# Optimization experiments

Hardware: AMD Instinct MI355X
Metric: run time of the kernel (lower is better)

## Reference

```python
import jax, jax.numpy as jnp
import numpy as np

ALPHA = 5.0   # ATan surrogate sharpness
THETA = 1.0   # firing threshold
EPS = 1e-5    # BatchNorm eps

@jax.custom_vjp
def spike(x):
    # forward: heaviside; backward: ATan surrogate
    return (x >= 0.0).astype(x.dtype)

def _spike_fwd(x):
    return spike(x), x

def _spike_bwd(x, g):
    return (g * (ALPHA / 2.0) / (1.0 + (jnp.pi / 2.0 * ALPHA * x) ** 2),)

spike.defvjp(_spike_fwd, _spike_bwd)

def lif_layer(x, W, beta_p, gamma, bias, U0):
    # x: [B,T,J], W: [I,J] -> h: [B,T,I]
    h = jnp.einsum('btj,ij->bti', x, W)
    # BatchNorm1d in training mode: per-channel stats over B*T (biased var)
    mu = h.mean(axis=(0, 1))
    var = h.var(axis=(0, 1))
    h = (h - mu) * jax.lax.rsqrt(var + EPS) * gamma + bias
    beta = jax.nn.sigmoid(beta_p)  # [I]
    S0 = jnp.zeros_like(U0)

    def step(carry, xt):
        Ut, St = carry
        Ut = beta * (Ut - THETA * St) + (1.0 - beta) * xt  # soft reset
        St = spike(Ut - THETA)
        return (Ut, St), St

    _, o = jax.lax.scan(step, (U0, S0), jnp.swapaxes(h, 0, 1))  # [T,B,I]
    return jnp.swapaxes(o, 0, 1)  # [B,T,I]

def setup_inputs() -> dict:
    key = jax.random.key(0)
    B, T, J, H = 32, 1024, 1024, 2048
    ks = jax.random.split(key, 16)
    f32 = jnp.float32
    inp = {
        'x': jax.random.normal(ks[0], (B, T, J), f32),
        'W1': jax.random.normal(ks[1], (H, J), f32) / np.sqrt(J),
        'beta1': jax.random.uniform(ks[2], (H,), f32, 0.0, 4.0),
        'gamma1': jnp.ones((H,), f32),
        'bias1': jnp.zeros((H,), f32),
        'U01': jax.random.uniform(ks[3], (B, H), f32),
        'W2': jax.random.normal(ks[4], (H, H), f32) / np.sqrt(H),
        'beta2': jax.random.uniform(ks[5], (H,), f32, 0.0, 4.0),
        'gamma2': jnp.ones((H,), f32),
        'bias2': jnp.zeros((H,), f32),
        'U02': jax.random.uniform(ks[6], (B, H), f32),
        'W3': jax.random.normal(ks[7], (J, H), f32) / np.sqrt(H),
        'beta3': jax.random.uniform(ks[8], (J,), f32, 0.0, 4.0),
        'gamma3': jnp.ones((J,), f32),
        'bias3': jnp.zeros((J,), f32),
        'U03': jax.random.uniform(ks[9], (B, J), f32),
    }
    return inp

def reference(x, W1, beta1, gamma1, bias1, U01,
              W2, beta2, gamma2, bias2, U02,
              W3, beta3, gamma3, bias3, U03):
    h = lif_layer(x, W1, beta1, gamma1, bias1, U01)
    h = lif_layer(h, W2, beta2, gamma2, bias2, U02)
    h = lif_layer(h, W3, beta3, gamma3, bias3, U03)
    return h
```

## Files before the change

### kernel.cpp

```cpp
#include <hip/hip_runtime.h>
#include <hip/hip_bf16.h>
#include <cmath>

#define BB 32
#define TT 1024
#define JJ 1024
#define HH 2048
#define MM (BB * TT)
#define MHALF (MM / 2)

typedef short s8v __attribute__((ext_vector_type(8)));
typedef float f4v __attribute__((ext_vector_type(4)));
typedef unsigned int u4v __attribute__((ext_vector_type(4)));
union ABu { u4v u; s8v v; };

__device__ inline void split_bf16x3(float w, unsigned short& h,
                                    unsigned short& m, unsigned short& l) {
    __hip_bfloat16 bh = __float2bfloat16(w);
    const float fh = __bfloat162float(bh);
    const float r1 = w - fh;
    __hip_bfloat16 bm = __float2bfloat16(r1);
    const float fm = __bfloat162float(bm);
    __hip_bfloat16 bl = __float2bfloat16(r1 - fm);
    h = *(unsigned short*)&bh; m = *(unsigned short*)&bm; l = *(unsigned short*)&bl;
}

__global__ void split_w(const float* __restrict__ W,
                        unsigned short* __restrict__ ph,
                        unsigned short* __restrict__ pm,
                        unsigned short* __restrict__ pl, int n)
{
    const int i = blockIdx.x * 256 + threadIdx.x;
    if (i >= n) return;
    split_bf16x3(W[i], ph[i], pm[i], pl[i]);
}

__global__ __launch_bounds__(256) void mfma_spk_gemm(
    const unsigned char* __restrict__ S,
    const unsigned short* __restrict__ Wh,
    const unsigned short* __restrict__ Wm,
    const unsigned short* __restrict__ Wl,
    float* __restrict__ C, int M, int N, int K)
{
    __shared__ __align__(16) unsigned short Blds[3][2][128][32];
    const int tid = threadIdx.x;
    const int wv = tid >> 6;
    const int lane = tid & 63;
    const int wm = wv >> 1, wn = wv & 1;
    const int r16 = lane & 15, quad = lane >> 4;
    const int bm = blockIdx.x * 128;
    const int bn = blockIdx.y * 128;
    const int Kb = K >> 3;

    f4v acc[4][4] = {};

    const int rl = lane >> 2, chl = lane & 3;
    size_t soff[2];
    int ldsrow[2];
#pragma unroll
    for (int i = 0; i < 2; ++i) {
        const int r = wv * 32 + i * 16 + rl;
        const int kc = (chl - (r >> 1)) & 3;
        soff[i] = (size_t)(bn + r) * K + kc * 8;
        ldsrow[i] = wv * 32 + i * 16;
    }

    size_t aoff[4];
#pragma unroll
    for (int ms = 0; ms < 4; ++ms)
        aoff[ms] = (size_t)(bm + wm * 64 + ms * 16 + r16) * Kb + quad;

    int bR[4], bC[4];
#pragma unroll
    for (int ns = 0; ns < 4; ++ns) {
        bR[ns] = wn * 64 + ns * 16 + r16;
        bC[ns] = ((quad + (bR[ns] >> 1)) & 3) * 8;
    }

    unsigned int ab[2][4];
#pragma unroll
    for (int kh = 0; kh < 2; ++kh)
#pragma unroll
        for (int ms = 0; ms < 4; ++ms) ab[kh][ms] = S[aoff[ms] + kh * 4];

    for (int k0 = 0; k0 < K; k0 += 64) {
        __syncthreads();
#pragma unroll
        for (int i = 0; i < 2; ++i)
#pragma unroll
            for (int kh = 0; kh < 2; ++kh) {
                __builtin_amdgcn_global_load_lds(
                    (const __attribute__((address_space(1))) void*)(Wh + soff[i] + k0 + kh * 32),
                    (__attribute__((address_space(3))) void*)&Blds[0][kh][ldsrow[i]][0], 16, 0, 0);
                __builtin_amdgcn_global_load_lds(
                    (const __attribute__((address_space(1))) void*)(Wm + soff[i] + k0 + kh * 32),
                    (__attribute__((address_space(3))) void*)&Blds[1][kh][ldsrow[i]][0], 16, 0, 0);
                __builtin_amdgcn_global_load_lds(
                    (const __attribute__((address_space(1))) void*)(Wl + soff[i] + k0 + kh * 32),
                    (__attribute__((address_space(3))) void*)&Blds[2][kh][ldsrow[i]][0], 16, 0, 0);
            }
        s8v afr[2][4];
#pragma unroll
        for (int kh = 0; kh < 2; ++kh)
#pragma unroll
            for (int ms = 0; ms < 4; ++ms) {
                ABu t;
                const unsigned int b = ab[kh][ms];
                t.u[0] = ((b        & 1u) * 0x3F80u) | (((b >> 1) & 1u) * 0x3F800000u);
                t.u[1] = (((b >> 2) & 1u) * 0x3F80u) | (((b >> 3) & 1u) * 0x3F800000u);
                t.u[2] = (((b >> 4) & 1u) * 0x3F80u) | (((b >> 5) & 1u) * 0x3F800000u);
                t.u[3] = (((b >> 6) & 1u) * 0x3F80u) | (((b >> 7) & 1u) * 0x3F800000u);
                afr[kh][ms] = t.v;
            }
        if (k0 + 64 < K) {
            const size_t kb = (size_t)((k0 + 64) >> 3);
#pragma unroll
            for (int kh = 0; kh < 2; ++kh)
#pragma unroll
                for (int ms = 0; ms < 4; ++ms) ab[kh][ms] = S[aoff[ms] + kb + kh * 4];
        }
        __syncthreads();
#pragma unroll
        for (int p = 0; p < 3; ++p)
#pragma unroll
            for (int kh = 0; kh < 2; ++kh) {
                s8v bf[4];
#pragma unroll
                for (int ns = 0; ns < 4; ++ns)
                    bf[ns] = *(const s8v*)&Blds[p][kh][bR[ns]][bC[ns]];
#pragma unroll
                for (int ms = 0; ms < 4; ++ms)
#pragma unroll
                    for (int ns = 0; ns < 4; ++ns)
                        acc[ms][ns] = __builtin_amdgcn_mfma_f32_16x16x32_bf16(
                            afr[kh][ms], bf[ns], acc[ms][ns], 0, 0, 0);
            }
    }

#pragma unroll
    for (int ms = 0; ms < 4; ++ms)
#pragma unroll
        for (int ns = 0; ns < 4; ++ns) {
            const int row = bm + wm * 64 + ms * 16 + quad * 4;
            const int col = bn + wn * 64 + ns * 16 + r16;
#pragma unroll
            for (int r = 0; r < 4; ++r)
                C[(size_t)(row + r) * N + col] = acc[ms][ns][r];
        }
}

struct Sp3 { unsigned int o0, o1, o2; };

__device__ inline Sp3 split_pair(float x, float y)
{
    const unsigned int xb = __float_as_uint(x), yb = __float_as_uint(y);
    const unsigned int x0 = xb & 0xFFFF0000u,  y0 = yb & 0xFFFF0000u;
    const float xr1 = x - __uint_as_float(x0), yr1 = y - __uint_as_float(y0);
    const unsigned int x1b = __float_as_uint(xr1), y1b = __float_as_uint(yr1);
    const unsigned int x1 = x1b & 0xFFFF0000u, y1 = y1b & 0xFFFF0000u;
    const float xr2 = xr1 - __uint_as_float(x1), yr2 = yr1 - __uint_as_float(y1);
    Sp3 r;
    r.o0 = __builtin_amdgcn_perm(yb, xb, 0x07060302u);
    r.o1 = __builtin_amdgcn_perm(y1b, x1b, 0x07060302u);
    r.o2 = __builtin_amdgcn_perm(__float_as_uint(yr2), __float_as_uint(xr2), 0x07060302u);
    return r;
}

__global__ __launch_bounds__(256) void mfma_f32x3_gemm(
    const float* __restrict__ A,
    const unsigned short* __restrict__ Wh,
    const unsigned short* __restrict__ Wm,
    const unsigned short* __restrict__ Wl,
    float* __restrict__ C, int M, int N, int K)
{
    __shared__ __align__(16) unsigned short Blds[3][2][128][32];
    const int tid = threadIdx.x;
    const int wv = tid >> 6;
    const int lane = tid & 63;
    const int wm = wv >> 1, wn = wv & 1;
    const int r16 = lane & 15, quad = lane >> 4;

    const int lin = blockIdx.y * 16 + blockIdx.x;
    const int ppx = gridDim.y >> 3;
    const int xcd = lin & 7, li = lin >> 3;
    const int pm = xcd * ppx + (li >> 4);
    const int pn = li & 15;
    const int bm = pm * 128;
    const int bn = pn * 128;

    f4v acc[4][4] = {};

    const int rl = lane >> 2, chl = lane & 3;
    size_t soff[2];
    int ldsrow[2];
#pragma unroll
    for (int i = 0; i < 2; ++i) {
        const int r = wv * 32 + i * 16 + rl;
        const int kc = (chl - (r >> 1)) & 3;
        soff[i] = (size_t)(bn + r) * K + kc * 8;
        ldsrow[i] = wv * 32 + i * 16;
    }

    size_t aoff[4];
#pragma unroll
    for (int ms = 0; ms < 4; ++ms)
        aoff[ms] = (size_t)(bm + wm * 64 + ms * 16 + r16) * K + quad * 8;

    int bR[4], bC[4];
#pragma unroll
    for (int ns = 0; ns < 4; ++ns) {
        bR[ns] = wn * 64 + ns * 16 + r16;
        bC[ns] = ((quad + (bR[ns] >> 1)) & 3) * 8;
    }

    float4 av[2][4][2];
#pragma unroll
    for (int kh = 0; kh < 2; ++kh)
#pragma unroll
        for (int ms = 0; ms < 4; ++ms) {
            av[kh][ms][0] = *(const float4*)(A + aoff[ms] + kh * 32);
            av[kh][ms][1] = *(const float4*)(A + aoff[ms] + kh * 32 + 4);
        }

    for (int k0 = 0; k0 < K; k0 += 64) {
        __syncthreads();
#pragma unroll
        for (int i = 0; i < 2; ++i)
#pragma unroll
            for (int kh = 0; kh < 2; ++kh) {
                __builtin_amdgcn_global_load_lds(
                    (const __attribute__((address_space(1))) void*)(Wh + soff[i] + k0 + kh * 32),
                    (__attribute__((address_space(3))) void*)&Blds[0][kh][ldsrow[i]][0], 16, 0, 0);
                __builtin_amdgcn_global_load_lds(
                    (const __attribute__((address_space(1))) void*)(Wm + soff[i] + k0 + kh * 32),
                    (__attribute__((address_space(3))) void*)&Blds[1][kh][ldsrow[i]][0], 16, 0, 0);
                __builtin_amdgcn_global_load_lds(
                    (const __attribute__((address_space(1))) void*)(Wl + soff[i] + k0 + kh * 32),
                    (__attribute__((address_space(3))) void*)&Blds[2][kh][ldsrow[i]][0], 16, 0, 0);
            }
        s8v afr[3][2][4];
#pragma unroll
        for (int kh = 0; kh < 2; ++kh)
#pragma unroll
            for (int ms = 0; ms < 4; ++ms) {
                ABu t0, t1, t2;
                const float4 v0 = av[kh][ms][0];
                const float4 v1 = av[kh][ms][1];
                const Sp3 s0 = split_pair(v0.x, v0.y);
                const Sp3 s1 = split_pair(v0.z, v0.w);
                const Sp3 s2 = split_pair(v1.x, v1.y);
                const Sp3 s3 = split_pair(v1.z, v1.w);
                t0.u[0] = s0.o0; t1.u[0] = s0.o1; t2.u[0] = s0.o2;
                t0.u[1] = s1.o0; t1.u[1] = s1.o1; t2.u[1] = s1.o2;
                t0.u[2] = s2.o0; t1.u[2] = s2.o1; t2.u[2] = s2.o2;
                t0.u[3] = s3.o0; t1.u[3] = s3.o1; t2.u[3] = s3.o2;
                afr[0][kh][ms] = t0.v;
                afr[1][kh][ms] = t1.v;
                afr[2][kh][ms] = t2.v;
            }
        __syncthreads();
        if (k0 + 64 < K) {
#pragma unroll
            for (int kh = 0; kh < 2; ++kh)
#pragma unroll
                for (int ms = 0; ms < 4; ++ms) {
                    av[kh][ms][0] = *(const float4*)(A + aoff[ms] + k0 + 64 + kh * 32);
                    av[kh][ms][1] = *(const float4*)(A + aoff[ms] + k0 + 64 + kh * 32 + 4);
                }
        }
#pragma unroll
        for (int kh = 0; kh < 2; ++kh)
#pragma unroll
            for (int pw = 0; pw < 3; ++pw) {
                s8v bf[4];
#pragma unroll
                for (int ns = 0; ns < 4; ++ns)
                    bf[ns] = *(const s8v*)&Blds[pw][kh][bR[ns]][bC[ns]];
#pragma unroll
                for (int pa = 0; pa + pw < 3; ++pa)
#pragma unroll
                    for (int ms = 0; ms < 4; ++ms)
#pragma unroll
                        for (int ns = 0; ns < 4; ++ns)
                            acc[ms][ns] = __builtin_amdgcn_mfma_f32_16x16x32_bf16(
                                afr[pa][kh][ms], bf[ns], acc[ms][ns], 0, 0, 0);
            }
    }

#pragma unroll
    for (int ms = 0; ms < 4; ++ms)
#pragma unroll
        for (int ns = 0; ns < 4; ++ns) {
            const int row = bm + wm * 64 + ms * 16 + quad * 4;
            const int col = bn + wn * 64 + ns * 16 + r16;
#pragma unroll
            for (int r = 0; r < 4; ++r)
                C[(size_t)(row + r) * N + col] = acc[ms][ns][r];
        }
}

#define RCHUNK 128

__global__ void bn_stats_partial2(const float* __restrict__ hA,
                                  const float* __restrict__ hB,
                                  float* __restrict__ partial, int N)
{
    const int n = blockIdx.x * 256 + threadIdx.x;
    const int chunk = blockIdx.y;
    const int half = (MM / RCHUNK) / 2;
    const float* __restrict__ h = (chunk < half) ? hA : hB;
    const int cl = chunk & (half - 1);
    const float* p = h + (size_t)cl * RCHUNK * N + n;
    float s = 0.f, s2 = 0.f;
#pragma unroll 4
    for (int r = 0; r < RCHUNK; ++r) {
        const float v = p[(size_t)r * N];
        s += v;
        s2 = fmaf(v, v, s2);
    }
    partial[((size_t)chunk * 2 + 0) * N + n] = s;
    partial[((size_t)chunk * 2 + 1) * N + n] = s2;
}

__global__ void bn_stats_final(const float* __restrict__ partial,
                               float* __restrict__ stats,
                               int N, int nchunks)
{
    const int n = blockIdx.x * 256 + threadIdx.x;
    double s = 0.0, s2 = 0.0;
    for (int c = 0; c < nchunks; ++c) {
        s  += (double)partial[((size_t)c * 2 + 0) * N + n];
        s2 += (double)partial[((size_t)c * 2 + 1) * N + n];
    }
    const double inv_m = 1.0 / (double)MM;
    const double mu = s * inv_m;
    const double var = s2 * inv_m - mu * mu;
    stats[n]     = (float)mu;
    stats[N + n] = (float)(1.0 / sqrt(var + 1e-5));
}

#define LIF_STEP_PACK(hv)                                            \
    do {                                                             \
        const float hn = ((hv) - mu) * rstd * g + bi;                \
        u = beta * (u - s) + omb * hn;                               \
        const bool sp = (u - 1.0f) >= 0.f;                           \
        s = sp ? 1.f : 0.f;                                          \
        const unsigned long long mball = __ballot(sp);               \
        if (lead) bits[widx] = mball;                                \
        widx += nw;                                                  \
    } while (0)

#define LIF_LOAD8(buf, tbase)                                        \
    _Pragma("unroll")                                                \
    for (int j = 0; j < 8; ++j) {                                    \
        const int tl = (tbase) + j;                                  \
        buf[j] = h[base + (size_t)(tl < TT ? tl : TT - 1) * N];      \
    }

__global__ __launch_bounds__(64) void bn_lif_scan_pack2(
    const float* __restrict__ hA,
    const float* __restrict__ hB,
    unsigned long long* __restrict__ bits,
    const float* __restrict__ stats,
    const float* __restrict__ gamma,
    const float* __restrict__ bias,
    const float* __restrict__ beta_p,
    const float* __restrict__ U0,
    int N)
{
    const int n = blockIdx.x * 64 + threadIdx.x;
    const int b = blockIdx.y;
    const float* __restrict__ h = (b < BB / 2) ? hA : hB;
    const int bl = b & (BB / 2 - 1);
    const int nw = N >> 6;
    const float mu = stats[n];
    const float rstd = stats[N + n];
    const float g = gamma[n];
    const float bi = bias[n];
    const float beta = 1.f / (1.f + expf(-beta_p[n]));
    const float omb = 1.f - beta;
    float u = U0[(size_t)b * N + n];
    float s = 0.f;
    const size_t base = ((size_t)bl * TT) * N + n;
    size_t widx = ((size_t)b * TT) * nw + (n >> 6);
    const bool lead = (threadIdx.x & 63) == 0;

    float b0[8], b1[8], b2[8], b3[8];
    LIF_LOAD8(b0, 0);
    LIF_LOAD8(b1, 8);
    LIF_LOAD8(b2, 16);
    for (int t0 = 0; t0 < TT; t0 += 32) {
        LIF_LOAD8(b3, t0 + 24);
#pragma unroll
        for (int j = 0; j < 8; ++j) { const float hv = b0[j]; LIF_STEP_PACK(hv); }
        LIF_LOAD8(b0, t0 + 32);
#pragma unroll
        for (int j = 0; j < 8; ++j) { const float hv = b1[j]; LIF_STEP_PACK(hv); }
        LIF_LOAD8(b1, t0 + 40);
#pragma unroll
        for (int j = 0; j < 8; ++j) { const float hv = b2[j]; LIF_STEP_PACK(hv); }
        LIF_LOAD8(b2, t0 + 48);
#pragma unroll
        for (int j = 0; j < 8; ++j) { const float hv = b3[j]; LIF_STEP_PACK(hv); }
    }
}

#define LIF_STEP_F32(hv)                                             \
    do {                                                             \
        const float hn = ((hv) - mu) * rstd * g + bi;                \
        u = beta * (u - s) + omb * hn;                               \
        s = ((u - 1.0f) >= 0.f) ? 1.f : 0.f;                         \
        out[oidx] = s;                                               \
        oidx += N;                                                   \
    } while (0)

__global__ __launch_bounds__(64) void bn_lif_scan_f32_2(
    const float* __restrict__ h,
    float* __restrict__ out,
    const float* __restrict__ stats,
    const float* __restrict__ gamma,
    const float* __restrict__ bias,
    const float* __restrict__ beta_p,
    const float* __restrict__ U0,
    int N)
{
    const int n = blockIdx.x * 64 + threadIdx.x;
    const int b = blockIdx.y;
    const float mu = stats[n];
    const float rstd = stats[N + n];
    const float g = gamma[n];
    const float bi = bias[n];
    const float beta = 1.f / (1.f + expf(-beta_p[n]));
    const float omb = 1.f - beta;
    float u = U0[(size_t)b * N + n];
    float s = 0.f;
    const size_t base = ((size_t)b * TT) * N + n;
    size_t oidx = base;

    float b0[8], b1[8], b2[8], b3[8];
    LIF_LOAD8(b0, 0);
    LIF_LOAD8(b1, 8);
    LIF_LOAD8(b2, 16);
    for (int t0 = 0; t0 < TT; t0 += 32) {
        LIF_LOAD8(b3, t0 + 24);
#pragma unroll
        for (int j = 0; j < 8; ++j) { const float hv = b0[j]; LIF_STEP_F32(hv); }
        LIF_LOAD8(b0, t0 + 32);
#pragma unroll
        for (int j = 0; j < 8; ++j) { const float hv = b1[j]; LIF_STEP_F32(hv); }
        LIF_LOAD8(b1, t0 + 40);
#pragma unroll
        for (int j = 0; j < 8; ++j) { const float hv = b2[j]; LIF_STEP_F32(hv); }
        LIF_LOAD8(b2, t0 + 48);
#pragma unroll
        for (int j = 0; j < 8; ++j) { const float hv = b3[j]; LIF_STEP_F32(hv); }
    }
}

extern "C" void kernel_launch(void* const* d_in, const int* in_sizes, int n_in,
                              void* d_out, int out_size, void* d_ws, size_t ws_size,
                              hipStream_t stream)
{
    const float* x   = (const float*)d_in[0];
    const float* W1  = (const float*)d_in[1];
    const float* bp1 = (const float*)d_in[2];
    const float* g1  = (const float*)d_in[3];
    const float* bi1 = (const float*)d_in[4];
    const float* U01 = (const float*)d_in[5];
    const float* W2  = (const float*)d_in[6];
    const float* bp2 = (const float*)d_in[7];
    const float* g2  = (const float*)d_in[8];
    const float* bi2 = (const float*)d_in[9];
    const float* U02 = (const float*)d_in[10];
    const float* W3  = (const float*)d_in[11];
    const float* bp3 = (const float*)d_in[12];
    const float* g3  = (const float*)d_in[13];
    const float* bi3 = (const float*)d_in[14];
    const float* U03 = (const float*)d_in[15];
    float* out = (float*)d_out;

    unsigned char* ws = (unsigned char*)d_ws;
    const size_t HA_BYTES  = (size_t)MHALF * HH * sizeof(float);
    const size_t SPK_BYTES = (size_t)MM * (HH / 8);
    float*              hA   = (float*)ws;
    float*              hB   = (float*)d_out;
    unsigned long long* spk  = (unsigned long long*)(ws + HA_BYTES);
    float*              part = (float*)(ws + HA_BYTES + SPK_BYTES);
    float*              stat = (float*)(ws + HA_BYTES + SPK_BYTES + 4194304);
    unsigned short*     W2h  = (unsigned short*)(ws + HA_BYTES + SPK_BYTES + 4194304 + 16384);
    unsigned short*     W2m  = W2h + (size_t)HH * HH;
    unsigned short*     W2l  = W2m + (size_t)HH * HH;
    unsigned short*     W3h  = W2l + (size_t)HH * HH;
    unsigned short*     W3m  = W3h + (size_t)JJ * HH;
    unsigned short*     W3l  = W3m + (size_t)JJ * HH;

    const dim3 blk(256);
    const dim3 blk64(64);
    const int nck = MM / RCHUNK;

    split_w<<<dim3((HH * JJ) / 256), blk, 0, stream>>>(W1, W2h, W2m, W2l, HH * JJ);
    mfma_f32x3_gemm<<<dim3(HH / 128, MHALF / 128), blk, 0, stream>>>(
        x, W2h, W2m, W2l, hA, MHALF, HH, JJ);
    mfma_f32x3_gemm<<<dim3(HH / 128, MHALF / 128), blk, 0, stream>>>(
        x + (size_t)MHALF * JJ, W2h, W2m, W2l, hB, MHALF, HH, JJ);
    split_w<<<dim3((HH * HH) / 256), blk, 0, stream>>>(W2, W2h, W2m, W2l, HH * HH);
    split_w<<<dim3((JJ * HH) / 256), blk, 0, stream>>>(W3, W3h, W3m, W3l, JJ * HH);

    bn_stats_partial2<<<dim3(HH / 256, nck), blk, 0, stream>>>(hA, hB, part, HH);
    bn_stats_final<<<dim3(HH / 256), blk, 0, stream>>>(part, stat, HH, nck);
    bn_lif_scan_pack2<<<dim3(HH / 64, BB), blk64, 0, stream>>>(
        hA, hB, spk, stat, g1, bi1, bp1, U01, HH);

    mfma_spk_gemm<<<dim3(MHALF / 128, HH / 128), blk, 0, stream>>>(
        (const unsigned char*)spk, W2h, W2m, W2l, hA, MHALF, HH, HH);
    mfma_spk_gemm<<<dim3(MHALF / 128, HH / 128), blk, 0, stream>>>(
        (const unsigned char*)spk + (size_t)MHALF * (HH / 8), W2h, W2m, W2l, hB, MHALF, HH, HH);
    bn_stats_partial2<<<dim3(HH / 256, nck), blk, 0, stream>>>(hA, hB, part, HH);
    bn_stats_final<<<dim3(HH / 256), blk, 0, stream>>>(part, stat, HH, nck);
    bn_lif_scan_pack2<<<dim3(HH / 64, BB), blk64, 0, stream>>>(
        hA, hB, spk, stat, g2, bi2, bp2, U02, HH);

    mfma_spk_gemm<<<dim3(MM / 128, JJ / 128), blk, 0, stream>>>(
        (const unsigned char*)spk, W3h, W3m, W3l, hA, MM, JJ, HH);
    bn_stats_partial2<<<dim3(JJ / 256, nck), blk, 0, stream>>>(
        hA, hA + (size_t)MHALF * JJ, part, JJ);
    bn_stats_final<<<dim3(JJ / 256), blk, 0, stream>>>(part, stat, JJ, nck);
    bn_lif_scan_f32_2<<<dim3(JJ / 64, BB), blk64, 0, stream>>>(
        hA, out, stat, g3, bi3, bp3, U03, JJ);
}
```

Measured before the change: 2.792 ms.

## Double-buffer weight tiles and enlarge spike GEMM block to 256 rows with 8 waves

The spike GEMM now uses 512 threads, so each block covers 256 M rows and eight waves share one 128-column weight tile, halving how often each weight tile is loaded. Weight slices are double-buffered in LDS and the next k-step is issued with global_load_lds during the current MFMAs. One of the two barriers per iteration is removed, and s_setprio raises wave priority around the MFMA bursts. The cost is twice the LDS footprint (48KB), possibly lower occupancy, and a reliance on a single barrier being enough to order the asynchronous LDS loads.

After: 2.703 ms. 1.03x faster.

```diff
diff --git a/kernel.cpp b/kernel.cpp
--- a/kernel.cpp
+++ b/kernel.cpp
@@ -35,35 +35,30 @@
     split_bf16x3(W[i], ph[i], pm[i], pl[i]);
 }
 
-__global__ __launch_bounds__(256) void mfma_spk_gemm(
+__global__ __launch_bounds__(512) void mfma_spk_gemm(
     const unsigned char* __restrict__ S,
     const unsigned short* __restrict__ Wh,
     const unsigned short* __restrict__ Wm,
     const unsigned short* __restrict__ Wl,
     float* __restrict__ C, int M, int N, int K)
 {
-    __shared__ __align__(16) unsigned short Blds[3][2][128][32];
+    __shared__ __align__(16) unsigned short Blds[2][3][2][128][32];
     const int tid = threadIdx.x;
     const int wv = tid >> 6;
     const int lane = tid & 63;
     const int wm = wv >> 1, wn = wv & 1;
     const int r16 = lane & 15, quad = lane >> 4;
-    const int bm = blockIdx.x * 128;
+    const int bm = blockIdx.x * 256;
     const int bn = blockIdx.y * 128;
     const int Kb = K >> 3;
 
     f4v acc[4][4] = {};
 
     const int rl = lane >> 2, chl = lane & 3;
-    size_t soff[2];
-    int ldsrow[2];
-#pragma unroll
-    for (int i = 0; i < 2; ++i) {
-        const int r = wv * 32 + i * 16 + rl;
-        const int kc = (chl - (r >> 1)) & 3;
-        soff[i] = (size_t)(bn + r) * K + kc * 8;
-        ldsrow[i] = wv * 32 + i * 16;
-    }
+    const int srow = wv * 16 + rl;
+    const int kc = (chl - (srow >> 1)) & 3;
+    const size_t soff = (size_t)(bn + srow) * K + kc * 8;
+    const int ldsrow = wv * 16;
 
     size_t aoff[4];
 #pragma unroll
@@ -77,49 +72,51 @@
         bC[ns] = ((quad + (bR[ns] >> 1)) & 3) * 8;
     }
 
+    auto stage = [&](int buf, int p, int kh, int k0) {
+        const unsigned short* Wp = (p == 0) ? Wh : (p == 1) ? Wm : Wl;
+        __builtin_amdgcn_global_load_lds(
+            (const __attribute__((address_space(1))) void*)(Wp + soff + k0 + kh * 32),
+            (__attribute__((address_space(3))) void*)&Blds[buf][p][kh][ldsrow][0], 16, 0, 0);
+    };
+
     unsigned int ab[2][4];
 #pragma unroll
     for (int kh = 0; kh < 2; ++kh)
 #pragma unroll
         for (int ms = 0; ms < 4; ++ms) ab[kh][ms] = S[aoff[ms] + kh * 4];
 
-    for (int k0 = 0; k0 < K; k0 += 64) {
+#pragma unroll
+    for (int p = 0; p < 3; ++p)
+#pragma unroll
+        for (int kh = 0; kh < 2; ++kh) stage(0, p, kh, 0);
+
+    const int NT = K >> 6;
+    for (int t = 0; t < NT; ++t) {
+        const int cur = t & 1, nxt = cur ^ 1;
+        const int k0 = t << 6;
         __syncthreads();
-#pragma unroll
-        for (int i = 0; i < 2; ++i)
-#pragma unroll
-            for (int kh = 0; kh < 2; ++kh) {
-                __builtin_amdgcn_global_load_lds(
-                    (const __attribute__((address_space(1))) void*)(Wh + soff[i] + k0 + kh * 32),
-                    (__attribute__((address_space(3))) void*)&Blds[0][kh][ldsrow[i]][0], 16, 0, 0);
-                __builtin_amdgcn_global_load_lds(
-                    (const __attribute__((address_space(1))) void*)(Wm + soff[i] + k0 + kh * 32),
-                    (__attribute__((address_space(3))) void*)&Blds[1][kh][ldsrow[i]][0], 16, 0, 0);
-                __builtin_amdgcn_global_load_lds(
-                    (const __attribute__((address_space(1))) void*)(Wl + soff[i] + k0 + kh * 32),
-                    (__attribute__((address_space(3))) void*)&Blds[2][kh][ldsrow[i]][0], 16, 0, 0);
+
+        s8v afr[2][4];
+#pragma unroll
+        for (int kh = 0; kh < 2; ++kh)
+#pragma unroll
+            for (int ms = 0; ms < 4; ++ms) {
+                ABu tu;
+                const unsigned int b = ab[kh][ms];
+                tu.u[0] = ((b        & 1u) * 0x3F80u) | (((b >> 1) & 1u) * 0x3F800000u);
+                tu.u[1] = (((b >> 2) & 1u) * 0x3F80u) | (((b >> 3) & 1u) * 0x3F800000u);
+                tu.u[2] = (((b >> 4) & 1u) * 0x3F80u) | (((b >> 5) & 1u) * 0x3F800000u);
+                tu.u[3] = (((b >> 6) & 1u) * 0x3F80u) | (((b >> 7) & 1u) * 0x3F800000u);
+                afr[kh][ms] = tu.v;
             }
-        s8v afr[2][4];
-#pragma unroll
-        for (int kh = 0; kh < 2; ++kh)
-#pragma unroll
-            for (int ms = 0; ms < 4; ++ms) {
-                ABu t;
-                const unsigned int b = ab[kh][ms];
-                t.u[0] = ((b        & 1u) * 0x3F80u) | (((b >> 1) & 1u) * 0x3F800000u);
-                t.u[1] = (((b >> 2) & 1u) * 0x3F80u) | (((b >> 3) & 1u) * 0x3F800000u);
-                t.u[2] = (((b >> 4) & 1u) * 0x3F80u) | (((b >> 5) & 1u) * 0x3F800000u);
-                t.u[3] = (((b >> 6) & 1u) * 0x3F80u) | (((b >> 7) & 1u) * 0x3F800000u);
-                afr[kh][ms] = t.v;
-            }
-        if (k0 + 64 < K) {
+        if (t + 1 < NT) {
             const size_t kb = (size_t)((k0 + 64) >> 3);
 #pragma unroll
             for (int kh = 0; kh < 2; ++kh)
 #pragma unroll
                 for (int ms = 0; ms < 4; ++ms) ab[kh][ms] = S[aoff[ms] + kb + kh * 4];
         }
-        __syncthreads();
+
 #pragma unroll
         for (int p = 0; p < 3; ++p)
 #pragma unroll
@@ -127,13 +124,16 @@
                 s8v bf[4];
 #pragma unroll
                 for (int ns = 0; ns < 4; ++ns)
-                    bf[ns] = *(const s8v*)&Blds[p][kh][bR[ns]][bC[ns]];
+                    bf[ns] = *(const s8v*)&Blds[cur][p][kh][bR[ns]][bC[ns]];
+                if (t + 1 < NT) stage(nxt, p, kh, k0 + 64);
+                __builtin_amdgcn_s_setprio(1);
 #pragma unroll
                 for (int ms = 0; ms < 4; ++ms)
 #pragma unroll
                     for (int ns = 0; ns < 4; ++ns)
                         acc[ms][ns] = __builtin_amdgcn_mfma_f32_16x16x32_bf16(
                             afr[kh][ms], bf[ns], acc[ms][ns], 0, 0, 0);
+                __builtin_amdgcn_s_setprio(0);
             }
     }
 
@@ -496,6 +496,7 @@
 
     const dim3 blk(256);
     const dim3 blk64(64);
+    const dim3 blk512(512);
     const int nck = MM / RCHUNK;
 
     split_w<<<dim3((HH * JJ) / 256), blk, 0, stream>>>(W1, W2h, W2m, W2l, HH * JJ);
@@ -511,16 +512,16 @@
     bn_lif_scan_pack2<<<dim3(HH / 64, BB), blk64, 0, stream>>>(
         hA, hB, spk, stat, g1, bi1, bp1, U01, HH);
 
-    mfma_spk_gemm<<<dim3(MHALF / 128, HH / 128), blk, 0, stream>>>(
+    mfma_spk_gemm<<<dim3(MHALF / 256, HH / 128), blk512, 0, stream>>>(
         (const unsigned char*)spk, W2h, W2m, W2l, hA, MHALF, HH, HH);
-    mfma_spk_gemm<<<dim3(MHALF / 128, HH / 128), blk, 0, stream>>>(
+    mfma_spk_gemm<<<dim3(MHALF / 256, HH / 128), blk512, 0, stream>>>(
         (const unsigned char*)spk + (size_t)MHALF * (HH / 8), W2h, W2m, W2l, hB, MHALF, HH, HH);
     bn_stats_partial2<<<dim3(HH / 256, nck), blk, 0, stream>>>(hA, hB, part, HH);
     bn_stats_final<<<dim3(HH / 256), blk, 0, stream>>>(part, stat, HH, nck);
     bn_lif_scan_pack2<<<dim3(HH / 64, BB), blk64, 0, stream>>>(
         hA, hB, spk, stat, g2, bi2, bp2, U02, HH);
 
-    mfma_spk_gemm<<<dim3(MM / 128, JJ / 128), blk, 0, stream>>>(
+    mfma_spk_gemm<<<dim3(MM / 256, JJ / 128), blk512, 0, stream>>>(
         (const unsigned char*)spk, W3h, W3m, W3l, hA, MM, JJ, HH);
     bn_stats_partial2<<<dim3(JJ / 256, nck), blk, 0, stream>>>(
         hA, hA + (size_t)MHALF * JJ, part, JJ);
```
